# Kernel tuning notes

Hardware: AMD Instinct MI355X
Metric: run time of the kernel (lower is better)

Reference implementation:

```python
import jax, jax.numpy as jnp
import numpy as np
import math

HIDDEN = 2048
N_HEADS = 32
N_KV_HEADS = 8
HEAD_DIM = HIDDEN // N_HEADS  # 64
N_REP = N_HEADS // N_KV_HEADS  # 4
ROPE_THETA = 10000.0
BSZ, SEQ = 2, 2048


def setup_inputs() -> dict:
    key = jax.random.key(0)
    ks = jax.random.split(key, 6)
    hidden_states = jax.random.normal(ks[0], (BSZ, SEQ, HIDDEN), dtype=jnp.float32)
    wq = jax.random.normal(ks[1], (HIDDEN, N_HEADS * HEAD_DIM), dtype=jnp.float32) * (HIDDEN ** -0.5)
    wk = jax.random.normal(ks[2], (HIDDEN, N_KV_HEADS * HEAD_DIM), dtype=jnp.float32) * (HIDDEN ** -0.5)
    wv = jax.random.normal(ks[3], (HIDDEN, N_KV_HEADS * HEAD_DIM), dtype=jnp.float32) * (HIDDEN ** -0.5)
    wo = jax.random.normal(ks[4], (N_HEADS * HEAD_DIM, HIDDEN), dtype=jnp.float32) * (HIDDEN ** -0.5)
    # additive causal mask [b, 1, q, kv]
    neg = jnp.finfo(jnp.float32).min
    causal = jnp.where(jnp.tril(jnp.ones((SEQ, SEQ), dtype=bool)), 0.0, neg)
    attention_mask = jnp.broadcast_to(causal[None, None], (BSZ, 1, SEQ, SEQ)).astype(jnp.float32)
    position_ids = jnp.broadcast_to(jnp.arange(SEQ, dtype=jnp.int32)[None], (BSZ, SEQ))
    return {
        "hidden_states": hidden_states,
        "wq": wq, "wk": wk, "wv": wv, "wo": wo,
        "attention_mask": attention_mask,
        "position_ids": position_ids,
    }


def _rope_cache(seq_len, dtype):
    inv_freq = 1.0 / (ROPE_THETA ** (jnp.arange(0, HEAD_DIM, 2, dtype=jnp.float32) / HEAD_DIM))
    t = jnp.arange(seq_len, dtype=jnp.float32)
    freqs = jnp.outer(t, inv_freq)              # [S, head_dim/2]
    emb = jnp.concatenate([freqs, freqs], -1)   # [S, head_dim]
    return jnp.cos(emb).astype(dtype), jnp.sin(emb).astype(dtype)


def _rotate_half(x):
    x1, x2 = jnp.split(x, 2, axis=-1)
    return jnp.concatenate([-x2, x1], axis=-1)


def reference(hidden_states, wq, wk, wv, wo, attention_mask, position_ids):
    b, s, _ = hidden_states.shape
    q = (hidden_states @ wq).reshape(b, s, N_HEADS, HEAD_DIM).transpose(0, 2, 1, 3)
    k = (hidden_states @ wk).reshape(b, s, N_KV_HEADS, HEAD_DIM).transpose(0, 2, 1, 3)
    v = (hidden_states @ wv).reshape(b, s, N_KV_HEADS, HEAD_DIM).transpose(0, 2, 1, 3)

    cos_c, sin_c = _rope_cache(s, hidden_states.dtype)
    cos = cos_c[position_ids][:, None]  # [b,1,s,head_dim]
    sin = sin_c[position_ids][:, None]
    q = q * cos + _rotate_half(q) * sin
    k = k * cos + _rotate_half(k) * sin

    # repeat_kv: [b, kvh, s, d] -> [b, kvh*n_rep, s, d]
    k = jnp.broadcast_to(k[:, :, None], (b, N_KV_HEADS, N_REP, s, HEAD_DIM)).reshape(b, N_HEADS, s, HEAD_DIM)
    v = jnp.broadcast_to(v[:, :, None], (b, N_KV_HEADS, N_REP, s, HEAD_DIM)).reshape(b, N_HEADS, s, HEAD_DIM)

    scores = jnp.einsum('bhqd,bhkd->bhqk', q, k) / math.sqrt(HEAD_DIM)
    scores = scores + attention_mask
    probs = jax.nn.softmax(scores.astype(jnp.float32), axis=-1).astype(q.dtype)
    attn = jnp.einsum('bhqk,bhkd->bhqd', probs, v)  # [b,h,s,d]
    attn = attn.transpose(0, 2, 1, 3).reshape(b, s, N_HEADS * HEAD_DIM)
    return attn @ wo
```

## Files before the change

kernel.cpp:

```cpp
#include <hip/hip_runtime.h>
#include <math.h>


typedef float f32x4 __attribute__((ext_vector_type(4)));
typedef short s16x8 __attribute__((ext_vector_type(8)));
typedef unsigned short u16x4 __attribute__((ext_vector_type(4)));

__device__ __forceinline__ unsigned short f2bf(float x) {
    union { float f; unsigned int u; } v; v.f = x;
    unsigned int r = v.u + 0x7FFF + ((v.u >> 16) & 1);
    return (unsigned short)(r >> 16);
}

__global__ __launch_bounds__(256) void prep(
    const float* __restrict__ X, const float* __restrict__ Wq,
    const float* __restrict__ Wk, const float* __restrict__ Wv,
    const float* __restrict__ Wo,
    unsigned short* __restrict__ Xb, unsigned short* __restrict__ Wqkvt,
    unsigned short* __restrict__ Wot) {
    const int bid = blockIdx.x;
    if (bid < 8192) {
        size_t i = (size_t)bid * 256 + threadIdx.x;
        f32x4 v = *(const f32x4*)&X[i * 4];
        u16x4 r;
        r[0] = f2bf(v[0]); r[1] = f2bf(v[1]); r[2] = f2bf(v[2]); r[3] = f2bf(v[3]);
        *(u16x4*)&Xb[i * 4] = r;
        return;
    }
    __shared__ float t[32][33];
    const int tb = bid - 8192;
    const int kbi = tb / 160, bx = tb - kbi * 160;
    const float* W; unsigned short* Out; int N, n0, nb;
    if (bx < 64)      { W = Wq; Out = Wqkvt; N = 2048; n0 = 0;    nb = bx; }
    else if (bx < 80) { W = Wk; Out = Wqkvt; N = 512;  n0 = 2048; nb = bx - 64; }
    else if (bx < 96) { W = Wv; Out = Wqkvt; N = 512;  n0 = 2560; nb = bx - 80; }
    else              { W = Wo; Out = Wot;   N = 2048; n0 = 0;    nb = bx - 96; }
    int kb = kbi * 32; nb *= 32;
    int tx = threadIdx.x & 31, ty = threadIdx.x >> 5;
#pragma unroll
    for (int i = 0; i < 4; ++i)
        t[ty + i * 8][tx] = W[(size_t)(kb + ty + i * 8) * N + nb + tx];
    __syncthreads();
#pragma unroll
    for (int i = 0; i < 4; ++i)
        Out[(size_t)(n0 + nb + ty + i * 8) * 2048 + kb + tx] = f2bf(t[tx][ty + i * 8]);
}

__global__ __launch_bounds__(256) void gemm_qkv_rope(
    const unsigned short* __restrict__ A, const unsigned short* __restrict__ Bt,
    const int* __restrict__ pos,
    unsigned short* __restrict__ Qb, unsigned short* __restrict__ Kb,
    unsigned short* __restrict__ Vb) {
    const int K = 2048;
    __shared__ unsigned short As[128 * 64];
    __shared__ unsigned short Bs[128 * 64];
    const int tid = threadIdx.x;
    const int wave = tid >> 6, lane = tid & 63;
    const int col = lane & 15, quad = lane >> 4;
    const int m0 = blockIdx.y * 128, n0 = blockIdx.x * 128;
    const int wm = (wave >> 1) * 64, wn = (wave & 1) * 64;

    const int lrow = lane >> 3;
    const int gch = (lane & 7) ^ lrow;
    const unsigned short* Ag = A + (size_t)(m0 + wave * 32 + lrow) * K + gch * 8;
    const unsigned short* Bg = Bt + (size_t)(n0 + wave * 32 + lrow) * K + gch * 8;
    unsigned short* AsW = As + wave * 2048;
    unsigned short* BsW = Bs + wave * 2048;

    f32x4 acc[4][4] = {};

    for (int k0 = 0; k0 < K; k0 += 64) {
#pragma unroll
        for (int i = 0; i < 4; ++i) {
            __builtin_amdgcn_global_load_lds(
                (const __attribute__((address_space(1))) void*)(Ag + (size_t)i * 8 * K + k0),
                (__attribute__((address_space(3))) void*)(AsW + i * 512), 16, 0, 0);
            __builtin_amdgcn_global_load_lds(
                (const __attribute__((address_space(1))) void*)(Bg + (size_t)i * 8 * K + k0),
                (__attribute__((address_space(3))) void*)(BsW + i * 512), 16, 0, 0);
        }
        __syncthreads();
#pragma unroll
        for (int ks = 0; ks < 2; ++ks) {
            const int slot = ((ks << 2) + quad) ^ (col & 7);
            s16x8 af[4], bf[4];
#pragma unroll
            for (int mi = 0; mi < 4; ++mi)
                af[mi] = *(const s16x8*)&As[(wm + mi * 16 + col) * 64 + slot * 8];
#pragma unroll
            for (int ni = 0; ni < 4; ++ni)
                bf[ni] = *(const s16x8*)&Bs[(wn + ni * 16 + col) * 64 + slot * 8];
#pragma unroll
            for (int mi = 0; mi < 4; ++mi)
#pragma unroll
                for (int ni = 0; ni < 4; ++ni)
                    acc[mi][ni] = __builtin_amdgcn_mfma_f32_16x16x32_bf16(
                        af[mi], bf[ni], acc[mi][ni], 0, 0, 0);
        }
        __syncthreads();
    }

    const int cb = n0 + wn;
    if (cb >= 2560) {
        const int hd = (cb - 2560) >> 6;
#pragma unroll
        for (int mi = 0; mi < 4; ++mi)
#pragma unroll
            for (int r = 0; r < 4; ++r) {
                int m = m0 + wm + mi * 16 + quad * 4 + r;
                int b = m >> 11, s = m & 2047;
                size_t rb = ((size_t)(b * 8 + hd) * 2048 + s) * 64;
#pragma unroll
                for (int ni = 0; ni < 4; ++ni)
                    Vb[rb + ni * 16 + col] = f2bf(acc[mi][ni][r]);
            }
    } else {
        const int isQ = (cb < 2048);
        const int hd = isQ ? (cb >> 6) : ((cb - 2048) >> 6);
        const int nh = isQ ? 32 : 8;
        const float scale = isQ ? 0.125f : 1.0f;
        unsigned short* Out = isQ ? Qb : Kb;
        const float NEG_LN_TH_32 = -0.28782313662425575f;
        const float inv0 = __expf((float)col * NEG_LN_TH_32);
        const float inv1 = __expf((float)(col + 16) * NEG_LN_TH_32);
#pragma unroll
        for (int mi = 0; mi < 4; ++mi)
#pragma unroll
            for (int r = 0; r < 4; ++r) {
                int m = m0 + wm + mi * 16 + quad * 4 + r;
                int b = m >> 11, s = m & 2047;
                float p = (float)pos[m];
                float sn0, cs0, sn1, cs1;
                __sincosf(p * inv0, &sn0, &cs0);
                __sincosf(p * inv1, &sn1, &cs1);
                float a0 = acc[mi][0][r], a1 = acc[mi][1][r];
                float b0 = acc[mi][2][r], b1 = acc[mi][3][r];
                size_t rb = ((size_t)(b * nh + hd) * 2048 + s) * 64;
                Out[rb + col]      = f2bf((a0 * cs0 - b0 * sn0) * scale);
                Out[rb + col + 16] = f2bf((a1 * cs1 - b1 * sn1) * scale);
                Out[rb + col + 32] = f2bf((b0 * cs0 + a0 * sn0) * scale);
                Out[rb + col + 48] = f2bf((b1 * cs1 + a1 * sn1) * scale);
            }
    }
}

__global__ __launch_bounds__(256) void gemm_bf16_nt(
    const unsigned short* __restrict__ A, const unsigned short* __restrict__ Bt,
    float* __restrict__ C, int K, int ldc) {
    __shared__ unsigned short As[128 * 64];
    __shared__ unsigned short Bs[128 * 64];
    const int tid = threadIdx.x;
    const int wave = tid >> 6, lane = tid & 63;
    const int col = lane & 15, quad = lane >> 4;
    const int m0 = blockIdx.y * 128, n0 = blockIdx.x * 128;
    const int wm = (wave >> 1) * 64, wn = (wave & 1) * 64;

    const int lrow = lane >> 3;
    const int gch = (lane & 7) ^ lrow;
    const unsigned short* Ag = A + (size_t)(m0 + wave * 32 + lrow) * K + gch * 8;
    const unsigned short* Bg = Bt + (size_t)(n0 + wave * 32 + lrow) * K + gch * 8;
    unsigned short* AsW = As + wave * 2048;
    unsigned short* BsW = Bs + wave * 2048;

    f32x4 acc[4][4] = {};

    for (int k0 = 0; k0 < K; k0 += 64) {
#pragma unroll
        for (int i = 0; i < 4; ++i) {
            __builtin_amdgcn_global_load_lds(
                (const __attribute__((address_space(1))) void*)(Ag + (size_t)i * 8 * K + k0),
                (__attribute__((address_space(3))) void*)(AsW + i * 512), 16, 0, 0);
            __builtin_amdgcn_global_load_lds(
                (const __attribute__((address_space(1))) void*)(Bg + (size_t)i * 8 * K + k0),
                (__attribute__((address_space(3))) void*)(BsW + i * 512), 16, 0, 0);
        }
        __syncthreads();
#pragma unroll
        for (int ks = 0; ks < 2; ++ks) {
            const int slot = ((ks << 2) + quad) ^ (col & 7);
            s16x8 af[4], bf[4];
#pragma unroll
            for (int mi = 0; mi < 4; ++mi)
                af[mi] = *(const s16x8*)&As[(wm + mi * 16 + col) * 64 + slot * 8];
#pragma unroll
            for (int ni = 0; ni < 4; ++ni)
                bf[ni] = *(const s16x8*)&Bs[(wn + ni * 16 + col) * 64 + slot * 8];
#pragma unroll
            for (int mi = 0; mi < 4; ++mi)
#pragma unroll
                for (int ni = 0; ni < 4; ++ni)
                    acc[mi][ni] = __builtin_amdgcn_mfma_f32_16x16x32_bf16(
                        af[mi], bf[ni], acc[mi][ni], 0, 0, 0);
        }
        __syncthreads();
    }
#pragma unroll
    for (int mi = 0; mi < 4; ++mi)
#pragma unroll
        for (int ni = 0; ni < 4; ++ni)
#pragma unroll
            for (int r = 0; r < 4; ++r) {
                int m = m0 + wm + mi * 16 + quad * 4 + r;
                int n = n0 + wn + ni * 16 + col;
                C[(size_t)m * ldc + n] = acc[mi][ni][r];
            }
}

__global__ __launch_bounds__(256) void transpose_v(
    const unsigned short* __restrict__ Vb, unsigned short* __restrict__ Vt) {
    __shared__ unsigned short t[64 * 66];
    const int bh = blockIdx.x >> 5, st = blockIdx.x & 31;
    const unsigned short* src = Vb + ((size_t)bh * 2048 + st * 64) * 64;
    unsigned short* dst = Vt + (size_t)bh * 64 * 2048 + st * 64;
    const int r = threadIdx.x >> 2, c = (threadIdx.x & 3) * 16;
    s16x8 v0 = *(const s16x8*)&src[r * 64 + c];
    s16x8 v1 = *(const s16x8*)&src[r * 64 + c + 8];
    unsigned* tw = (unsigned*)&t[r * 66 + c];
#pragma unroll
    for (int q2 = 0; q2 < 4; ++q2) tw[q2] = ((unsigned*)&v0)[q2];
#pragma unroll
    for (int q2 = 0; q2 < 4; ++q2) tw[4 + q2] = ((unsigned*)&v1)[q2];
    __syncthreads();
    const int d = threadIdx.x >> 2, sc2 = (threadIdx.x & 3) * 16;
    unsigned short outv[16];
#pragma unroll
    for (int jj = 0; jj < 16; ++jj) outv[jj] = t[(sc2 + jj) * 66 + d];
    *(s16x8*)&dst[(size_t)d * 2048 + sc2] = *(s16x8*)&outv[0];
    *(s16x8*)&dst[(size_t)d * 2048 + sc2 + 8] = *(s16x8*)&outv[8];
}

__global__ __launch_bounds__(128, 2) void flash_attn(
    const unsigned short* __restrict__ Qb, const unsigned short* __restrict__ Kb,
    const unsigned short* __restrict__ Vt, unsigned short* __restrict__ Ob) {
    __shared__ unsigned short Ks[64 * 64];
    __shared__ unsigned short Vs[64 * 64];
    __shared__ unsigned short PsA[2][32 * 64];
    __shared__ unsigned short PsB[2][32 * 64];

    const int tid = threadIdx.x;
    const int wave = tid >> 6, lane = tid & 63;
    const int col = lane & 15, quad = lane >> 4;

    const int id = blockIdx.x;
    const int j = ((id & 15) + ((id >> 8) << 2)) & 15;
    const int bh = id >> 4;
    const int b = bh >> 5, h = bh & 31, kvh = h >> 2;
    const int qA0 = (31 - j) * 64, qB0 = j * 64;
    const int qwA = qA0 + wave * 32, qwB = qB0 + wave * 32;

    const unsigned short* Qg  = Qb + ((size_t)(b * 32 + h) * 2048) * 64;
    const unsigned short* Kgb = Kb + ((size_t)(b * 8 + kvh) * 2048) * 64;
    const unsigned short* Vgb = Vt + ((size_t)(b * 8 + kvh) * 64) * 2048;

    const int r8 = lane >> 3, g = (lane & 7) ^ r8;
    const unsigned short* KgL = Kgb + (size_t)(wave * 32 + r8) * 64 + g * 8;
    const unsigned short* VgL = Vgb + (size_t)(wave * 32 + r8) * 2048 + g * 8;
    unsigned short* KsW = Ks + wave * 32 * 64;
    unsigned short* VsW = Vs + wave * 32 * 64;

    const s16x8 onesf = {16256, 16256, 16256, 16256, 16256, 16256, 16256, 16256};

    s16x8 qfA[2][2], qfB[2][2];
#pragma unroll
    for (int qc = 0; qc < 2; ++qc)
#pragma unroll
        for (int ks = 0; ks < 2; ++ks) {
            qfA[qc][ks] = *(const s16x8*)&Qg[(size_t)(qwA + qc * 16 + col) * 64 + ks * 32 + quad * 8];
            qfB[qc][ks] = *(const s16x8*)&Qg[(size_t)(qwB + qc * 16 + col) * 64 + ks * 32 + quad * 8];
        }

    f32x4 aoA[2][4] = {}, aoB[2][4] = {};
    f32x4 alA[2] = {}, alB[2] = {};

    for (int kv0 = 0; kv0 <= qA0; kv0 += 64) {
#pragma unroll
        for (int i = 0; i < 4; ++i) {
            __builtin_amdgcn_global_load_lds(
                (const __attribute__((address_space(1))) void*)(KgL + (size_t)(kv0 + i * 8) * 64),
                (__attribute__((address_space(3))) void*)(KsW + i * 512), 16, 0, 0);
            __builtin_amdgcn_global_load_lds(
                (const __attribute__((address_space(1))) void*)(VgL + kv0 + (size_t)i * 8 * 2048),
                (__attribute__((address_space(3))) void*)(VsW + i * 512), 16, 0, 0);
        }
        __syncthreads();
        const bool doB = (kv0 <= qB0);
#pragma unroll
        for (int mi = 0; mi < 4; ++mi) {
            const int s0 = quad ^ (col & 7);
            const int s1 = (4 + quad) ^ (col & 7);
            s16x8 kf0 = *(const s16x8*)&Ks[(mi * 16 + col) * 64 + s0 * 8];
            s16x8 kf1 = *(const s16x8*)&Ks[(mi * 16 + col) * 64 + s1 * 8];
            const int chl = (mi * 2 + (quad >> 1)) ^ (col & 7);
#pragma unroll
            for (int qc = 0; qc < 2; ++qc) {
                f32x4 sc = {};
                sc = __builtin_amdgcn_mfma_f32_16x16x32_bf16(kf0, qfA[qc][0], sc, 0, 0, 0);
                sc = __builtin_amdgcn_mfma_f32_16x16x32_bf16(kf1, qfA[qc][1], sc, 0, 0, 0);
                if (kv0 == qA0) {
                    int kvb = kv0 + mi * 16 + quad * 4, q = qwA + qc * 16 + col;
#pragma unroll
                    for (int r = 0; r < 4; ++r)
                        if (kvb + r > q) sc[r] = -1e30f;
                }
                unsigned eb[4];
#pragma unroll
                for (int r = 0; r < 4; ++r) eb[r] = __float_as_uint(__expf(sc[r]));
                uint2 pk;
                pk.x = __builtin_amdgcn_perm(eb[1], eb[0], 0x07060302u);
                pk.y = __builtin_amdgcn_perm(eb[3], eb[2], 0x07060302u);
                *(uint2*)&PsA[wave][(qc * 16 + col) * 64 + chl * 8 + (quad & 1) * 4] = pk;
            }
            if (doB) {
#pragma unroll
                for (int qc = 0; qc < 2; ++qc) {
                    f32x4 sc = {};
                    sc = __builtin_amdgcn_mfma_f32_16x16x32_bf16(kf0, qfB[qc][0], sc, 0, 0, 0);
                    sc = __builtin_amdgcn_mfma_f32_16x16x32_bf16(kf1, qfB[qc][1], sc, 0, 0, 0);
                    if (kv0 == qB0) {
                        int kvb = kv0 + mi * 16 + quad * 4, q = qwB + qc * 16 + col;
#pragma unroll
                        for (int r = 0; r < 4; ++r)
                            if (kvb + r > q) sc[r] = -1e30f;
                    }
                    unsigned eb[4];
#pragma unroll
                    for (int r = 0; r < 4; ++r) eb[r] = __float_as_uint(__expf(sc[r]));
                    uint2 pk;
                    pk.x = __builtin_amdgcn_perm(eb[1], eb[0], 0x07060302u);
                    pk.y = __builtin_amdgcn_perm(eb[3], eb[2], 0x07060302u);
                    *(uint2*)&PsB[wave][(qc * 16 + col) * 64 + chl * 8 + (quad & 1) * 4] = pk;
                }
            }
        }
        asm volatile("s_waitcnt lgkmcnt(0)" ::: "memory");
#pragma unroll
        for (int ks = 0; ks < 2; ++ks) {
            const int slot = ((ks << 2) + quad) ^ (col & 7);
            s16x8 vf[4];
#pragma unroll
            for (int di = 0; di < 4; ++di)
                vf[di] = *(const s16x8*)&Vs[(di * 16 + col) * 64 + slot * 8];
#pragma unroll
            for (int qc = 0; qc < 2; ++qc) {
                s16x8 pfA = *(const s16x8*)&PsA[wave][(qc * 16 + col) * 64 + slot * 8];
                alA[qc] = __builtin_amdgcn_mfma_f32_16x16x32_bf16(pfA, onesf, alA[qc], 0, 0, 0);
#pragma unroll
                for (int di = 0; di < 4; ++di)
                    aoA[qc][di] = __builtin_amdgcn_mfma_f32_16x16x32_bf16(pfA, vf[di], aoA[qc][di], 0, 0, 0);
            }
            if (doB) {
#pragma unroll
                for (int qc = 0; qc < 2; ++qc) {
                    s16x8 pfB = *(const s16x8*)&PsB[wave][(qc * 16 + col) * 64 + slot * 8];
                    alB[qc] = __builtin_amdgcn_mfma_f32_16x16x32_bf16(pfB, onesf, alB[qc], 0, 0, 0);
#pragma unroll
                    for (int di = 0; di < 4; ++di)
                        aoB[qc][di] = __builtin_amdgcn_mfma_f32_16x16x32_bf16(pfB, vf[di], aoB[qc][di], 0, 0, 0);
                }
            }
        }
        __syncthreads();
    }

#pragma unroll
    for (int qc = 0; qc < 2; ++qc)
#pragma unroll
        for (int r = 0; r < 4; ++r) {
            {
                int qg = qwA + qc * 16 + quad * 4 + r;
                float inv = 1.f / alA[qc][r];
                size_t base = ((size_t)b * 2048 + qg) * 2048 + h * 64;
#pragma unroll
                for (int di = 0; di < 4; ++di)
                    Ob[base + di * 16 + col] = f2bf(aoA[qc][di][r] * inv);
            }
            {
                int qg = qwB + qc * 16 + quad * 4 + r;
                float inv = 1.f / alB[qc][r];
                size_t base = ((size_t)b * 2048 + qg) * 2048 + h * 64;
#pragma unroll
                for (int di = 0; di < 4; ++di)
                    Ob[base + di * 16 + col] = f2bf(aoB[qc][di][r] * inv);
            }
        }
}

extern "C" void kernel_launch(void* const* d_in, const int* in_sizes, int n_in,
                              void* d_out, int out_size, void* d_ws, size_t ws_size,
                              hipStream_t stream) {
    const float* X  = (const float*)d_in[0];
    const float* Wq = (const float*)d_in[1];
    const float* Wk = (const float*)d_in[2];
    const float* Wv = (const float*)d_in[3];
    const float* Wo = (const float*)d_in[4];
    const int* pos  = (const int*)d_in[6];
    float* out = (float*)d_out;

    char* ws = (char*)d_ws;
    unsigned short* Xb    = (unsigned short*)(ws + 0);
    unsigned short* Wqkvt = (unsigned short*)(ws + 16777216);
    unsigned short* Wot   = (unsigned short*)(ws + 29360128);
    unsigned short* Qb    = (unsigned short*)(ws + 37748736);
    unsigned short* Kb    = (unsigned short*)(ws + 54525952);
    unsigned short* Vb    = (unsigned short*)(ws + 58720256);
    unsigned short* Vt    = (unsigned short*)(ws + 62914560);
    unsigned short* Attn  = Xb;

    prep<<<18432, 256, 0, stream>>>(X, Wq, Wk, Wv, Wo, Xb, Wqkvt, Wot);
    gemm_qkv_rope<<<dim3(24, 32), 256, 0, stream>>>(Xb, Wqkvt, pos, Qb, Kb, Vb);
    transpose_v<<<512, 256, 0, stream>>>(Vb, Vt);
    flash_attn<<<1024, 128, 0, stream>>>(Qb, Kb, Vt, Attn);
    gemm_bf16_nt<<<dim3(16, 32), 256, 0, stream>>>(Attn, Wot, out, 2048, 2048);
}
```

Baseline: 316.3 us.

## Rewrite QKV GEMM with 256x256 tiles, double-buffered LDS and interleaved prefetch

Replaces the 128x128, 4-wave QKV projection GEMM with a 256x256 tile, 8-wave kernel whose waves each compute 128x64. It double-buffers LDS and splits each k-step into four MFMA quadrants, issuing the async global-to-LDS loads for upcoming tiles between them under explicit waitcnt, barriers and setprio. The aim is to raise data reuse per loaded byte and hide global load latency behind MFMA work. In exchange it uses 128KB of LDS and many more accumulator registers, and launches only 192 blocks, which may underfill the GPU's CUs.

```diff
diff --git a/kernel.cpp b/kernel.cpp
--- a/kernel.cpp
+++ b/kernel.cpp
@@ -46,65 +46,154 @@
         Out[(size_t)(n0 + nb + ty + i * 8) * 2048 + kb + tx] = f2bf(t[tx][ty + i * 8]);
 }
 
-__global__ __launch_bounds__(256) void gemm_qkv_rope(
+__global__ __launch_bounds__(512, 2) void gemm_qkv_rope(
     const unsigned short* __restrict__ A, const unsigned short* __restrict__ Bt,
     const int* __restrict__ pos,
     unsigned short* __restrict__ Qb, unsigned short* __restrict__ Kb,
     unsigned short* __restrict__ Vb) {
     const int K = 2048;
-    __shared__ unsigned short As[128 * 64];
-    __shared__ unsigned short Bs[128 * 64];
+    const int NKT = 32;
+    __shared__ unsigned short As[2][256 * 64];
+    __shared__ unsigned short Bs[2][256 * 64];
     const int tid = threadIdx.x;
     const int wave = tid >> 6, lane = tid & 63;
     const int col = lane & 15, quad = lane >> 4;
-    const int m0 = blockIdx.y * 128, n0 = blockIdx.x * 128;
-    const int wm = (wave >> 1) * 64, wn = (wave & 1) * 64;
+    const int m0 = blockIdx.y * 256, n0 = blockIdx.x * 256;
+    const int wm = (wave >> 2) * 128, wn = (wave & 3) * 64;
 
     const int lrow = lane >> 3;
     const int gch = (lane & 7) ^ lrow;
-    const unsigned short* Ag = A + (size_t)(m0 + wave * 32 + lrow) * K + gch * 8;
-    const unsigned short* Bg = Bt + (size_t)(n0 + wave * 32 + lrow) * K + gch * 8;
-    unsigned short* AsW = As + wave * 2048;
-    unsigned short* BsW = Bs + wave * 2048;
-
-    f32x4 acc[4][4] = {};
-
-    for (int k0 = 0; k0 < K; k0 += 64) {
-#pragma unroll
-        for (int i = 0; i < 4; ++i) {
-            __builtin_amdgcn_global_load_lds(
-                (const __attribute__((address_space(1))) void*)(Ag + (size_t)i * 8 * K + k0),
-                (__attribute__((address_space(3))) void*)(AsW + i * 512), 16, 0, 0);
-            __builtin_amdgcn_global_load_lds(
-                (const __attribute__((address_space(1))) void*)(Bg + (size_t)i * 8 * K + k0),
-                (__attribute__((address_space(3))) void*)(BsW + i * 512), 16, 0, 0);
-        }
-        __syncthreads();
-#pragma unroll
-        for (int ks = 0; ks < 2; ++ks) {
-            const int slot = ((ks << 2) + quad) ^ (col & 7);
-            s16x8 af[4], bf[4];
-#pragma unroll
-            for (int mi = 0; mi < 4; ++mi)
-                af[mi] = *(const s16x8*)&As[(wm + mi * 16 + col) * 64 + slot * 8];
-#pragma unroll
-            for (int ni = 0; ni < 4; ++ni)
-                bf[ni] = *(const s16x8*)&Bs[(wn + ni * 16 + col) * 64 + slot * 8];
-#pragma unroll
-            for (int mi = 0; mi < 4; ++mi)
-#pragma unroll
-                for (int ni = 0; ni < 4; ++ni)
-                    acc[mi][ni] = __builtin_amdgcn_mfma_f32_16x16x32_bf16(
-                        af[mi], bf[ni], acc[mi][ni], 0, 0, 0);
-        }
-        __syncthreads();
-    }
+    const unsigned short* Ag = A + (size_t)(m0 + lrow) * K + gch * 8;
+    const unsigned short* Bg = Bt + (size_t)(n0 + lrow) * K + gch * 8;
+    const int rbA0 = wave * 8;
+    const int rbB0 = ((wave >> 2) << 6) + (wave & 3) * 8;
+
+#define STAGE_A(buf, h, kt)                                                    \
+    {                                                                          \
+        _Pragma("unroll")                                                      \
+        for (int l = 0; l < 2; ++l) {                                          \
+            const int rb = (h) * 64 + l * 128 + rbA0;                          \
+            __builtin_amdgcn_global_load_lds(                                  \
+                (const __attribute__((address_space(1))) void*)(Ag + (size_t)rb * K + (size_t)(kt) * 64), \
+                (__attribute__((address_space(3))) void*)(&As[buf][rb * 64]),  \
+                16, 0, 0);                                                     \
+        }                                                                      \
+    }
+#define STAGE_B(buf, h, kt)                                                    \
+    {                                                                          \
+        _Pragma("unroll")                                                      \
+        for (int l = 0; l < 2; ++l) {                                          \
+            const int rb = (h) * 32 + l * 128 + rbB0;                          \
+            __builtin_amdgcn_global_load_lds(                                  \
+                (const __attribute__((address_space(1))) void*)(Bg + (size_t)rb * K + (size_t)(kt) * 64), \
+                (__attribute__((address_space(3))) void*)(&Bs[buf][rb * 64]),  \
+                16, 0, 0);                                                     \
+        }                                                                      \
+    }
+#define RD_A(buf, mi, ks)                                                      \
+    (*(const s16x8*)&As[buf][(wm + (mi) * 16 + col) * 64 +                     \
+                             ((((ks) << 2) + quad) ^ (col & 7)) * 8])
+#define RD_B(buf, ni, ks)                                                      \
+    (*(const s16x8*)&Bs[buf][(wn + (ni) * 16 + col) * 64 +                     \
+                             ((((ks) << 2) + quad) ^ (col & 7)) * 8])
+
+    s16x8 a[4][2], bl[2][2], bh[2][2];
+    f32x4 acc[8][4] = {};
+
+    STAGE_A(0, 0, 0); STAGE_B(0, 0, 0); STAGE_B(0, 1, 0); STAGE_A(0, 1, 0);
+    STAGE_A(1, 0, 1); STAGE_B(1, 0, 1); STAGE_B(1, 1, 1);
+    asm volatile("s_waitcnt vmcnt(6)" ::: "memory");
+    __builtin_amdgcn_s_barrier();
+
+    for (int t = 0; t < NKT; ++t) {
+        const int p = t & 1;
+#pragma unroll
+        for (int mi = 0; mi < 4; ++mi) {
+            a[mi][0] = RD_A(p, mi, 0);
+            a[mi][1] = RD_A(p, mi, 1);
+        }
+#pragma unroll
+        for (int ni = 0; ni < 2; ++ni) {
+            bl[ni][0] = RD_B(p, ni, 0);
+            bl[ni][1] = RD_B(p, ni, 1);
+        }
+        if (t + 1 < NKT) STAGE_A(p ^ 1, 1, t + 1);
+        __builtin_amdgcn_s_barrier();
+        asm volatile("s_waitcnt lgkmcnt(0)" ::: "memory");
+        __builtin_amdgcn_s_setprio(1);
+#pragma unroll
+        for (int mi = 0; mi < 4; ++mi)
+#pragma unroll
+            for (int ni = 0; ni < 2; ++ni) {
+                acc[mi][ni] = __builtin_amdgcn_mfma_f32_16x16x32_bf16(a[mi][0], bl[ni][0], acc[mi][ni], 0, 0, 0);
+                acc[mi][ni] = __builtin_amdgcn_mfma_f32_16x16x32_bf16(a[mi][1], bl[ni][1], acc[mi][ni], 0, 0, 0);
+            }
+        __builtin_amdgcn_s_setprio(0);
+        __builtin_amdgcn_s_barrier();
+#pragma unroll
+        for (int ni = 0; ni < 2; ++ni) {
+            bh[ni][0] = RD_B(p, 2 + ni, 0);
+            bh[ni][1] = RD_B(p, 2 + ni, 1);
+        }
+        if (t + 2 < NKT) STAGE_A(p, 0, t + 2);
+        __builtin_amdgcn_s_barrier();
+        asm volatile("s_waitcnt lgkmcnt(0)" ::: "memory");
+        __builtin_amdgcn_s_setprio(1);
+#pragma unroll
+        for (int mi = 0; mi < 4; ++mi)
+#pragma unroll
+            for (int ni = 0; ni < 2; ++ni) {
+                acc[mi][2 + ni] = __builtin_amdgcn_mfma_f32_16x16x32_bf16(a[mi][0], bh[ni][0], acc[mi][2 + ni], 0, 0, 0);
+                acc[mi][2 + ni] = __builtin_amdgcn_mfma_f32_16x16x32_bf16(a[mi][1], bh[ni][1], acc[mi][2 + ni], 0, 0, 0);
+            }
+        __builtin_amdgcn_s_setprio(0);
+        __builtin_amdgcn_s_barrier();
+#pragma unroll
+        for (int mi = 0; mi < 4; ++mi) {
+            a[mi][0] = RD_A(p, 4 + mi, 0);
+            a[mi][1] = RD_A(p, 4 + mi, 1);
+        }
+        if (t + 2 < NKT) STAGE_B(p, 0, t + 2);
+        __builtin_amdgcn_s_barrier();
+        asm volatile("s_waitcnt lgkmcnt(0)" ::: "memory");
+        __builtin_amdgcn_s_setprio(1);
+#pragma unroll
+        for (int mi = 0; mi < 4; ++mi)
+#pragma unroll
+            for (int ni = 0; ni < 2; ++ni) {
+                acc[4 + mi][2 + ni] = __builtin_amdgcn_mfma_f32_16x16x32_bf16(a[mi][0], bh[ni][0], acc[4 + mi][2 + ni], 0, 0, 0);
+                acc[4 + mi][2 + ni] = __builtin_amdgcn_mfma_f32_16x16x32_bf16(a[mi][1], bh[ni][1], acc[4 + mi][2 + ni], 0, 0, 0);
+            }
+        __builtin_amdgcn_s_setprio(0);
+        __builtin_amdgcn_s_barrier();
+        if (t + 2 < NKT) STAGE_B(p, 1, t + 2);
+        if (t + 2 < NKT) {
+            asm volatile("s_waitcnt vmcnt(6)" ::: "memory");
+        } else {
+            asm volatile("s_waitcnt vmcnt(0)" ::: "memory");
+        }
+        __builtin_amdgcn_s_barrier();
+        __builtin_amdgcn_s_setprio(1);
+#pragma unroll
+        for (int mi = 0; mi < 4; ++mi)
+#pragma unroll
+            for (int ni = 0; ni < 2; ++ni) {
+                acc[4 + mi][ni] = __builtin_amdgcn_mfma_f32_16x16x32_bf16(a[mi][0], bl[ni][0], acc[4 + mi][ni], 0, 0, 0);
+                acc[4 + mi][ni] = __builtin_amdgcn_mfma_f32_16x16x32_bf16(a[mi][1], bl[ni][1], acc[4 + mi][ni], 0, 0, 0);
+            }
+        __builtin_amdgcn_s_setprio(0);
+        __builtin_amdgcn_s_barrier();
+    }
+#undef STAGE_A
+#undef STAGE_B
+#undef RD_A
+#undef RD_B
 
     const int cb = n0 + wn;
     if (cb >= 2560) {
         const int hd = (cb - 2560) >> 6;
 #pragma unroll
-        for (int mi = 0; mi < 4; ++mi)
+        for (int mi = 0; mi < 8; ++mi)
 #pragma unroll
             for (int r = 0; r < 4; ++r) {
                 int m = m0 + wm + mi * 16 + quad * 4 + r;
@@ -124,7 +213,7 @@
         const float inv0 = __expf((float)col * NEG_LN_TH_32);
         const float inv1 = __expf((float)(col + 16) * NEG_LN_TH_32);
 #pragma unroll
-        for (int mi = 0; mi < 4; ++mi)
+        for (int mi = 0; mi < 8; ++mi)
 #pragma unroll
             for (int r = 0; r < 4; ++r) {
                 int m = m0 + wm + mi * 16 + quad * 4 + r;
@@ -407,7 +496,7 @@
     unsigned short* Attn  = Xb;
 
     prep<<<18432, 256, 0, stream>>>(X, Wq, Wk, Wv, Wo, Xb, Wqkvt, Wot);
-    gemm_qkv_rope<<<dim3(24, 32), 256, 0, stream>>>(Xb, Wqkvt, pos, Qb, Kb, Vb);
+    gemm_qkv_rope<<<dim3(12, 16), 512, 0, stream>>>(Xb, Wqkvt, pos, Qb, Kb, Vb);
     transpose_v<<<512, 256, 0, stream>>>(Vb, Vt);
     flash_attn<<<1024, 128, 0, stream>>>(Qb, Kb, Vt, Attn);
     gemm_bf16_nt<<<dim3(16, 32), 256, 0, stream>>>(Attn, Wot, out, 2048, 2048);
```

Result: no change. 317.7 us (+0.4%).

## Double-buffer QKV GEMM with 128x192 tiles, fuse V transpose, XCD-aware block swizzle

Applied to the files above, without the earlier changes.

The QKV+RoPE GEMM is rebuilt with 384-thread blocks on 128x192 tiles, double-buffered LDS loaded asynchronously two k-tiles ahead, explicit waitcnt/barrier scheduling and setprio around MFMA bursts. The V epilogue writes the transposed layout directly, so the separate transpose_v kernel and its extra global round trip go away. Both GEMMs also remap block indices so neighbouring tiles land on the same XCD for better L2 reuse. The cost is more LDS per block (80KB), a hand-tuned vmcnt count that must match the number of issued loads, and strided 8-byte V stores.

```diff
diff --git a/kernel.cpp b/kernel.cpp
--- a/kernel.cpp
+++ b/kernel.cpp
@@ -46,74 +46,124 @@
         Out[(size_t)(n0 + nb + ty + i * 8) * 2048 + kb + tx] = f2bf(t[tx][ty + i * 8]);
 }
 
-__global__ __launch_bounds__(256) void gemm_qkv_rope(
+__global__ __launch_bounds__(384, 3) void gemm_qkv_rope(
     const unsigned short* __restrict__ A, const unsigned short* __restrict__ Bt,
     const int* __restrict__ pos,
     unsigned short* __restrict__ Qb, unsigned short* __restrict__ Kb,
-    unsigned short* __restrict__ Vb) {
+    unsigned short* __restrict__ Vt) {
     const int K = 2048;
-    __shared__ unsigned short As[128 * 64];
-    __shared__ unsigned short Bs[128 * 64];
+    const int NKT = 32;
+    __shared__ unsigned short As[2][128 * 64];
+    __shared__ unsigned short Bs[2][192 * 64];
     const int tid = threadIdx.x;
     const int wave = tid >> 6, lane = tid & 63;
     const int col = lane & 15, quad = lane >> 4;
-    const int m0 = blockIdx.y * 128, n0 = blockIdx.x * 128;
-    const int wm = (wave >> 1) * 64, wn = (wave & 1) * 64;
+
+    const int lin = blockIdx.y * 16 + blockIdx.x;
+    const int xcd = lin & 7, t8 = lin >> 3;
+    const int bx = (xcd & 1) * 8 + (t8 & 7);
+    const int by = (xcd >> 1) * 8 + (t8 >> 3);
+    const int m0 = by * 128, n0 = bx * 192;
+    const int wrow = wave / 3, wcol = wave - wrow * 3;
+    const int wm = wrow * 64, wn = wcol * 64;
 
     const int lrow = lane >> 3;
     const int gch = (lane & 7) ^ lrow;
-    const unsigned short* Ag = A + (size_t)(m0 + wave * 32 + lrow) * K + gch * 8;
-    const unsigned short* Bg = Bt + (size_t)(n0 + wave * 32 + lrow) * K + gch * 8;
-    unsigned short* AsW = As + wave * 2048;
-    unsigned short* BsW = Bs + wave * 2048;
-
+    const unsigned short* Ag = A + (size_t)(m0 + lrow) * K + gch * 8;
+    const unsigned short* Bg = Bt + (size_t)(n0 + lrow) * K + gch * 8;
+
+    const int aid0 = wave, aid1 = wave + 6;
+    const int aid2 = (wave + 12 < 16) ? wave + 12 : wave - 4;
+
+#define STAGE_T(buf, kt)                                                       \
+    {                                                                          \
+        __builtin_amdgcn_global_load_lds(                                      \
+            (const __attribute__((address_space(1))) void*)(Ag + (size_t)aid0 * 8 * K + (size_t)(kt) * 64), \
+            (__attribute__((address_space(3))) void*)(&As[buf][aid0 * 512]), 16, 0, 0); \
+        __builtin_amdgcn_global_load_lds(                                      \
+            (const __attribute__((address_space(1))) void*)(Ag + (size_t)aid1 * 8 * K + (size_t)(kt) * 64), \
+            (__attribute__((address_space(3))) void*)(&As[buf][aid1 * 512]), 16, 0, 0); \
+        __builtin_amdgcn_global_load_lds(                                      \
+            (const __attribute__((address_space(1))) void*)(Ag + (size_t)aid2 * 8 * K + (size_t)(kt) * 64), \
+            (__attribute__((address_space(3))) void*)(&As[buf][aid2 * 512]), 16, 0, 0); \
+        _Pragma("unroll")                                                      \
+        for (int j = 0; j < 4; ++j) {                                          \
+            const int bid = wave + j * 6;                                      \
+            __builtin_amdgcn_global_load_lds(                                  \
+                (const __attribute__((address_space(1))) void*)(Bg + (size_t)bid * 8 * K + (size_t)(kt) * 64), \
+                (__attribute__((address_space(3))) void*)(&Bs[buf][bid * 512]), 16, 0, 0); \
+        }                                                                      \
+    }
+#define RD_A(buf, mi, ks)                                                      \
+    (*(const s16x8*)&As[buf][(wm + (mi) * 16 + col) * 64 +                     \
+                             ((((ks) << 2) + quad) ^ (col & 7)) * 8])
+#define RD_B(buf, ni, ks)                                                      \
+    (*(const s16x8*)&Bs[buf][(wn + (ni) * 16 + col) * 64 +                     \
+                             ((((ks) << 2) + quad) ^ (col & 7)) * 8])
+
+    s16x8 a[2][2], b[4][2];
     f32x4 acc[4][4] = {};
 
-    for (int k0 = 0; k0 < K; k0 += 64) {
-#pragma unroll
-        for (int i = 0; i < 4; ++i) {
-            __builtin_amdgcn_global_load_lds(
-                (const __attribute__((address_space(1))) void*)(Ag + (size_t)i * 8 * K + k0),
-                (__attribute__((address_space(3))) void*)(AsW + i * 512), 16, 0, 0);
-            __builtin_amdgcn_global_load_lds(
-                (const __attribute__((address_space(1))) void*)(Bg + (size_t)i * 8 * K + k0),
-                (__attribute__((address_space(3))) void*)(BsW + i * 512), 16, 0, 0);
-        }
-        __syncthreads();
-#pragma unroll
-        for (int ks = 0; ks < 2; ++ks) {
-            const int slot = ((ks << 2) + quad) ^ (col & 7);
-            s16x8 af[4], bf[4];
-#pragma unroll
-            for (int mi = 0; mi < 4; ++mi)
-                af[mi] = *(const s16x8*)&As[(wm + mi * 16 + col) * 64 + slot * 8];
-#pragma unroll
-            for (int ni = 0; ni < 4; ++ni)
-                bf[ni] = *(const s16x8*)&Bs[(wn + ni * 16 + col) * 64 + slot * 8];
-#pragma unroll
-            for (int mi = 0; mi < 4; ++mi)
-#pragma unroll
-                for (int ni = 0; ni < 4; ++ni)
-                    acc[mi][ni] = __builtin_amdgcn_mfma_f32_16x16x32_bf16(
-                        af[mi], bf[ni], acc[mi][ni], 0, 0, 0);
-        }
-        __syncthreads();
-    }
+    STAGE_T(0, 0);
+    STAGE_T(1, 1);
+    asm volatile("s_waitcnt vmcnt(7)" ::: "memory");
+    __builtin_amdgcn_s_barrier();
+
+    for (int t = 0; t < NKT; ++t) {
+        const int p = t & 1;
+#pragma unroll
+        for (int mi = 0; mi < 2; ++mi) { a[mi][0] = RD_A(p, mi, 0); a[mi][1] = RD_A(p, mi, 1); }
+#pragma unroll
+        for (int ni = 0; ni < 4; ++ni) { b[ni][0] = RD_B(p, ni, 0); b[ni][1] = RD_B(p, ni, 1); }
+        __builtin_amdgcn_s_barrier();
+        asm volatile("s_waitcnt lgkmcnt(0)" ::: "memory");
+        __builtin_amdgcn_s_setprio(1);
+#pragma unroll
+        for (int mi = 0; mi < 2; ++mi)
+#pragma unroll
+            for (int ni = 0; ni < 4; ++ni) {
+                acc[mi][ni] = __builtin_amdgcn_mfma_f32_16x16x32_bf16(a[mi][0], b[ni][0], acc[mi][ni], 0, 0, 0);
+                acc[mi][ni] = __builtin_amdgcn_mfma_f32_16x16x32_bf16(a[mi][1], b[ni][1], acc[mi][ni], 0, 0, 0);
+            }
+        __builtin_amdgcn_s_setprio(0);
+        __builtin_amdgcn_s_barrier();
+#pragma unroll
+        for (int mi = 0; mi < 2; ++mi) { a[mi][0] = RD_A(p, 2 + mi, 0); a[mi][1] = RD_A(p, 2 + mi, 1); }
+        __builtin_amdgcn_s_barrier();
+        asm volatile("s_waitcnt lgkmcnt(0)" ::: "memory");
+        if (t + 2 < NKT) STAGE_T(p, t + 2);
+        __builtin_amdgcn_s_setprio(1);
+#pragma unroll
+        for (int mi = 0; mi < 2; ++mi)
+#pragma unroll
+            for (int ni = 0; ni < 4; ++ni) {
+                acc[2 + mi][ni] = __builtin_amdgcn_mfma_f32_16x16x32_bf16(a[mi][0], b[ni][0], acc[2 + mi][ni], 0, 0, 0);
+                acc[2 + mi][ni] = __builtin_amdgcn_mfma_f32_16x16x32_bf16(a[mi][1], b[ni][1], acc[2 + mi][ni], 0, 0, 0);
+            }
+        __builtin_amdgcn_s_setprio(0);
+        if (t + 2 < NKT) asm volatile("s_waitcnt vmcnt(7)" ::: "memory");
+        else             asm volatile("s_waitcnt vmcnt(0)" ::: "memory");
+        __builtin_amdgcn_s_barrier();
+    }
+#undef STAGE_T
+#undef RD_A
+#undef RD_B
 
     const int cb = n0 + wn;
     if (cb >= 2560) {
         const int hd = (cb - 2560) >> 6;
 #pragma unroll
-        for (int mi = 0; mi < 4; ++mi)
-#pragma unroll
-            for (int r = 0; r < 4; ++r) {
-                int m = m0 + wm + mi * 16 + quad * 4 + r;
-                int b = m >> 11, s = m & 2047;
-                size_t rb = ((size_t)(b * 8 + hd) * 2048 + s) * 64;
-#pragma unroll
-                for (int ni = 0; ni < 4; ++ni)
-                    Vb[rb + ni * 16 + col] = f2bf(acc[mi][ni][r]);
-            }
+        for (int mi = 0; mi < 4; ++mi) {
+            int mb = m0 + wm + mi * 16 + quad * 4;
+            int b = mb >> 11, s0 = mb & 2047;
+#pragma unroll
+            for (int ni = 0; ni < 4; ++ni) {
+                u16x4 v;
+#pragma unroll
+                for (int r = 0; r < 4; ++r) v[r] = f2bf(acc[mi][ni][r]);
+                *(u16x4*)&Vt[((size_t)(b * 8 + hd) * 64 + ni * 16 + col) * 2048 + s0] = v;
+            }
+        }
     } else {
         const int isQ = (cb < 2048);
         const int hd = isQ ? (cb >> 6) : ((cb - 2048) >> 6);
@@ -152,7 +202,11 @@
     const int tid = threadIdx.x;
     const int wave = tid >> 6, lane = tid & 63;
     const int col = lane & 15, quad = lane >> 4;
-    const int m0 = blockIdx.y * 128, n0 = blockIdx.x * 128;
+    const int lin = blockIdx.y * 16 + blockIdx.x;
+    const int xcd = lin & 7, t6 = lin >> 3;
+    const int bx = (xcd & 1) * 8 + (t6 & 7);
+    const int by = (xcd >> 1) * 8 + (t6 >> 3);
+    const int m0 = by * 128, n0 = bx * 128;
     const int wm = (wave >> 1) * 64, wn = (wave & 1) * 64;
 
     const int lrow = lane >> 3;
@@ -204,29 +258,6 @@
                 int n = n0 + wn + ni * 16 + col;
                 C[(size_t)m * ldc + n] = acc[mi][ni][r];
             }
-}
-
-__global__ __launch_bounds__(256) void transpose_v(
-    const unsigned short* __restrict__ Vb, unsigned short* __restrict__ Vt) {
-    __shared__ unsigned short t[64 * 66];
-    const int bh = blockIdx.x >> 5, st = blockIdx.x & 31;
-    const unsigned short* src = Vb + ((size_t)bh * 2048 + st * 64) * 64;
-    unsigned short* dst = Vt + (size_t)bh * 64 * 2048 + st * 64;
-    const int r = threadIdx.x >> 2, c = (threadIdx.x & 3) * 16;
-    s16x8 v0 = *(const s16x8*)&src[r * 64 + c];
-    s16x8 v1 = *(const s16x8*)&src[r * 64 + c + 8];
-    unsigned* tw = (unsigned*)&t[r * 66 + c];
-#pragma unroll
-    for (int q2 = 0; q2 < 4; ++q2) tw[q2] = ((unsigned*)&v0)[q2];
-#pragma unroll
-    for (int q2 = 0; q2 < 4; ++q2) tw[4 + q2] = ((unsigned*)&v1)[q2];
-    __syncthreads();
-    const int d = threadIdx.x >> 2, sc2 = (threadIdx.x & 3) * 16;
-    unsigned short outv[16];
-#pragma unroll
-    for (int jj = 0; jj < 16; ++jj) outv[jj] = t[(sc2 + jj) * 66 + d];
-    *(s16x8*)&dst[(size_t)d * 2048 + sc2] = *(s16x8*)&outv[0];
-    *(s16x8*)&dst[(size_t)d * 2048 + sc2 + 8] = *(s16x8*)&outv[8];
 }
 
 __global__ __launch_bounds__(128, 2) void flash_attn(
@@ -402,13 +433,11 @@
     unsigned short* Wot   = (unsigned short*)(ws + 29360128);
     unsigned short* Qb    = (unsigned short*)(ws + 37748736);
     unsigned short* Kb    = (unsigned short*)(ws + 54525952);
-    unsigned short* Vb    = (unsigned short*)(ws + 58720256);
     unsigned short* Vt    = (unsigned short*)(ws + 62914560);
     unsigned short* Attn  = Xb;
 
     prep<<<18432, 256, 0, stream>>>(X, Wq, Wk, Wv, Wo, Xb, Wqkvt, Wot);
-    gemm_qkv_rope<<<dim3(24, 32), 256, 0, stream>>>(Xb, Wqkvt, pos, Qb, Kb, Vb);
-    transpose_v<<<512, 256, 0, stream>>>(Vb, Vt);
+    gemm_qkv_rope<<<dim3(16, 32), 384, 0, stream>>>(Xb, Wqkvt, pos, Qb, Kb, Vt);
     flash_attn<<<1024, 128, 0, stream>>>(Qb, Kb, Vt, Attn);
     gemm_bf16_nt<<<dim3(16, 32), 256, 0, stream>>>(Attn, Wot, out, 2048, 2048);
 }
```

New measurement: 318.0 us. No clear change (+0.5%).
